# Optimization experiments

Hardware: AMD Instinct MI355X
Metric: run time of the kernel (lower is better)

## Reference

```python
import jax, jax.numpy as jnp
import numpy as np

JACCARD_THRESH = 0.5
NEGPOS_RATIO = 3
VAR = (0.1, 0.2)


def point_form(p):
    # center-size (cx,cy,w,h) -> corner (xmin,ymin,xmax,ymax)
    return jnp.concatenate([p[:, :2] - p[:, 2:] / 2, p[:, :2] + p[:, 2:] / 2], axis=1)


def jaccard(a, b):
    # a: [No,4] corner boxes, b: [Np,4] corner boxes -> IoU [No,Np]
    lt = jnp.maximum(a[:, None, :2], b[None, :, :2])
    rb = jnp.minimum(a[:, None, 2:], b[None, :, 2:])
    wh = jnp.clip(rb - lt, 0.0)
    inter = wh[..., 0] * wh[..., 1]
    area_a = ((a[:, 2] - a[:, 0]) * (a[:, 3] - a[:, 1]))[:, None]
    area_b = ((b[:, 2] - b[:, 0]) * (b[:, 3] - b[:, 1]))[None, :]
    return inter / (area_a + area_b - inter)


def encode(matched, priors):
    # matched: [Np,4] corner GT, priors: [Np,4] center-size
    g_cxcy = ((matched[:, :2] + matched[:, 2:]) / 2 - priors[:, :2]) / (VAR[0] * priors[:, 2:])
    g_wh = jnp.log((matched[:, 2:] - matched[:, :2]) / priors[:, 2:]) / VAR[1]
    return jnp.concatenate([g_cxcy, g_wh], axis=1)


def match_one(truths, labels, priors):
    # truths: [No,4], labels: [No], priors: [Np,4] center-size
    overlaps = jaccard(truths, point_form(priors))          # [No,Np]
    best_prior_idx = jnp.argmax(overlaps, axis=1)           # [No]
    best_truth_overlap = jnp.max(overlaps, axis=0)          # [Np]
    best_truth_idx = jnp.argmax(overlaps, axis=0)           # [Np]
    # each GT keeps its best prior (overlap forced to 2)
    best_truth_overlap = best_truth_overlap.at[best_prior_idx].set(2.0)
    best_truth_idx = best_truth_idx.at[best_prior_idx].set(jnp.arange(truths.shape[0]))
    matched = truths[best_truth_idx]                        # [Np,4]
    conf = labels[best_truth_idx].astype(jnp.int32) + 1     # background = 0
    conf = jnp.where(best_truth_overlap < JACCARD_THRESH, 0, conf)
    return encode(matched, priors), conf


def reference(loc_data, conf_data, dbox_list, targets):
    num_batch, num_dbox, num_classes = conf_data.shape
    truths = targets[:, :, :4]
    labels = targets[:, :, 4]
    loc_t, conf_t = jax.vmap(match_one, in_axes=(0, 0, None))(truths, labels, dbox_list)
    pos_mask = conf_t > 0                                   # [B,Np]
    # localization loss: SmoothL1 (beta=1), summed over positive dboxes
    diff = loc_data - loc_t
    ad = jnp.abs(diff)
    sl1 = jnp.where(ad < 1.0, 0.5 * diff * diff, ad - 0.5)
    loss_l = jnp.sum(sl1 * pos_mask[..., None].astype(sl1.dtype))
    # per-dbox cross entropy
    logp = jax.nn.log_softmax(conf_data, axis=-1)
    ce = -jnp.take_along_axis(logp, conf_t[..., None], axis=-1)[..., 0]  # [B,Np]
    # hard negative mining: rank (descending) of pos-zeroed CE via double argsort
    loss_c_hnm = jnp.where(pos_mask, 0.0, ce)
    loss_idx = jnp.argsort(-loss_c_hnm, axis=1)
    idx_rank = jnp.argsort(loss_idx, axis=1)
    num_pos = jnp.sum(pos_mask, axis=1, keepdims=True)      # [B,1]
    num_neg = jnp.minimum(num_pos * NEGPOS_RATIO, num_dbox)
    neg_mask = idx_rank < num_neg
    sel = jnp.logical_or(pos_mask, neg_mask)
    loss_c = jnp.sum(jnp.where(sel, ce, 0.0))
    N = jnp.sum(num_pos).astype(loss_l.dtype)
    return loss_l / N, loss_c / N


def setup_inputs() -> dict:
    key = jax.random.key(0)
    ks = jax.random.split(key, 7)
    B, Np, C, No = 128, 8732, 21, 16
    loc_data = jax.random.normal(ks[0], (B, Np, 4), dtype=jnp.float32) * 0.1
    conf_data = jax.random.normal(ks[1], (B, Np, C), dtype=jnp.float32)
    # default boxes in center-size form, w/h strictly positive
    cxcy = jax.random.uniform(ks[2], (Np, 2), minval=0.05, maxval=0.95)
    wh = jax.random.uniform(ks[3], (Np, 2), minval=0.05, maxval=0.5)
    dbox_list = jnp.concatenate([cxcy, wh], axis=1).astype(jnp.float32)
    # ground truth: valid corner-form boxes + class label in [0,20)
    gcxcy = jax.random.uniform(ks[4], (B, No, 2), minval=0.2, maxval=0.8)
    gwh = jax.random.uniform(ks[5], (B, No, 2), minval=0.05, maxval=0.3)
    boxes = jnp.concatenate([gcxcy - gwh / 2, gcxcy + gwh / 2], axis=-1)
    lab = jax.random.randint(ks[6], (B, No, 1), 0, C - 1).astype(jnp.float32)
    targets = jnp.concatenate([boxes, lab], axis=-1).astype(jnp.float32)
    return {"loc_data": loc_data, "conf_data": conf_data, "dbox_list": dbox_list, "targets": targets}
```

## Files before the change

### kernel.cpp

```cpp
#include <hip/hip_runtime.h>
#include <stdint.h>

#define TPB 256
#define SELTPB 1024
#define SELWAVES (SELTPB / 64)
#define MAXNO 64
#define NMB 16

__device__ __forceinline__ float sl1f(float d) {
    float ad = fabsf(d);
    return ad < 1.0f ? 0.5f * d * d : ad - 0.5f;
}

__device__ __forceinline__ float iou_pair(float tx1, float ty1, float tx2, float ty2, float ta,
                                          float px1, float py1, float px2, float py2, float pa) {
    float ltx = fmaxf(tx1, px1), lty = fmaxf(ty1, py1);
    float rbx = fminf(tx2, px2), rby = fminf(ty2, py2);
    float wx = fmaxf(rbx - ltx, 0.0f), wy = fmaxf(rby - lty, 0.0f);
    float inter = wx * wy;
    return inter / ((ta + pa) - inter);
}

template <int NO>
__global__ __launch_bounds__(256) void match_partial_kernel(
    const float* __restrict__ dbox, const float* __restrict__ targets,
    unsigned long long* __restrict__ pkeys, int Np, int No) {
    int b = blockIdx.y, mb = blockIdx.x;
    int tid = threadIdx.x;
    __shared__ float s_t[NO][5];
    __shared__ unsigned long long s_k[4][NO];
    if (tid < No) {
        const float* tr = targets + ((size_t)b * No + tid) * 5;
        float x1 = tr[0], y1 = tr[1], x2 = tr[2], y2 = tr[3];
        s_t[tid][0] = x1; s_t[tid][1] = y1; s_t[tid][2] = x2; s_t[tid][3] = y2;
        s_t[tid][4] = (x2 - x1) * (y2 - y1);
    }
    __syncthreads();
    int clen = (Np + NMB - 1) / NMB;
    int start = mb * clen;
    int end = start + clen;
    if (end > Np) end = Np;
    unsigned long long key[NO];
#pragma unroll
    for (int t = 0; t < NO; ++t) key[t] = 0ull;
    for (int p = start + tid; p < end; p += 256) {
        float4 pr = *reinterpret_cast<const float4*>(dbox + (size_t)p * 4);
        float px1 = pr.x - pr.z * 0.5f, py1 = pr.y - pr.w * 0.5f;
        float px2 = pr.x + pr.z * 0.5f, py2 = pr.y + pr.w * 0.5f;
        float pa = (px2 - px1) * (py2 - py1);
        unsigned lowp = 0xFFFFFFFFu - (unsigned)p;
#pragma unroll
        for (int t = 0; t < NO; ++t) {
            float iou = iou_pair(s_t[t][0], s_t[t][1], s_t[t][2], s_t[t][3], s_t[t][4],
                                 px1, py1, px2, py2, pa);
            unsigned long long k =
                (((unsigned long long)__float_as_uint(iou)) << 32) | (unsigned long long)lowp;
            if (k > key[t]) key[t] = k;
        }
    }
    int lane = tid & 63, wv = tid >> 6;
#pragma unroll
    for (int t = 0; t < NO; ++t) {
        unsigned long long k = key[t];
        for (int off = 32; off; off >>= 1) {
            unsigned long long o = __shfl_down(k, off);
            if (o > k) k = o;
        }
        if (lane == 0) s_k[wv][t] = k;
    }
    __syncthreads();
    if (tid < No) {
        unsigned long long m = s_k[0][tid];
#pragma unroll
        for (int w = 1; w < 4; ++w)
            if (s_k[w][tid] > m) m = s_k[w][tid];
        pkeys[((size_t)b * NMB + mb) * No + tid] = m;
    }
}

template <int CC>
__global__ __launch_bounds__(TPB) void main_kernel(
    const float* __restrict__ loc, const float* __restrict__ conf,
    const float* __restrict__ dbox, const float* __restrict__ targets,
    const unsigned long long* __restrict__ pkeys,
    float* __restrict__ v, float* __restrict__ part_l, float* __restrict__ part_c,
    int* __restrict__ part_n, int Np, int C, int No, int nchunk) {
    extern __shared__ float s_conf[];
    __shared__ float s_t[MAXNO][5];
    __shared__ float s_lab[MAXNO];
    __shared__ int s_ovr[MAXNO];
    __shared__ float s_red1[4];
    __shared__ float s_red2[4];
    __shared__ int s_redi[4];
    int b = blockIdx.y, chunk = blockIdx.x, tid = threadIdx.x;
    int p = chunk * TPB + tid;
    bool valid = p < Np;
    if (tid < No) {
        const float* tr = targets + ((size_t)b * No + tid) * 5;
        float x1 = tr[0], y1 = tr[1], x2 = tr[2], y2 = tr[3];
        s_t[tid][0] = x1; s_t[tid][1] = y1; s_t[tid][2] = x2; s_t[tid][3] = y2;
        s_t[tid][4] = (x2 - x1) * (y2 - y1);
        s_lab[tid] = tr[4];
        unsigned long long k = pkeys[((size_t)b * NMB + 0) * No + tid];
        for (int m = 1; m < NMB; ++m) {
            unsigned long long kk = pkeys[((size_t)b * NMB + m) * No + tid];
            if (kk > k) k = kk;
        }
        s_ovr[tid] = (int)(0xFFFFFFFFu - (unsigned)(k & 0xFFFFFFFFull));
    }
    int pbase = chunk * TPB;
    int cnt = Np - pbase;
    if (cnt > TPB) cnt = TPB;
    const float* cbase = conf + ((size_t)b * Np + (size_t)pbase) * C;
    {
        int ntot = cnt * C;
        int nv4 = ntot >> 2;
        const float4* c4 = reinterpret_cast<const float4*>(cbase);
        float4* s4 = reinterpret_cast<float4*>(s_conf);
        for (int i = tid; i < nv4; i += TPB) s4[i] = c4[i];
        for (int i = (nv4 << 2) + tid; i < ntot; i += TPB) s_conf[i] = cbase[i];
    }
    __syncthreads();

    float lossl = 0.0f, posce = 0.0f;
    int npos = 0;
    if (valid) {
        float4 pr = *reinterpret_cast<const float4*>(dbox + (size_t)p * 4);
        float px1 = pr.x - pr.z * 0.5f, py1 = pr.y - pr.w * 0.5f;
        float px2 = pr.x + pr.z * 0.5f, py2 = pr.y + pr.w * 0.5f;
        float pa = (px2 - px1) * (py2 - py1);
        float bov = -1.0f;
        int bidx = 0;
        for (int t = 0; t < No; ++t) {
            float iou = iou_pair(s_t[t][0], s_t[t][1], s_t[t][2], s_t[t][3], s_t[t][4],
                                 px1, py1, px2, py2, pa);
            if (iou > bov) { bov = iou; bidx = t; }
        }
        for (int t = 0; t < No; ++t)
            if (s_ovr[t] == p) { bidx = t; bov = 2.0f; }
        int ct = (bov < 0.5f) ? 0 : ((int)s_lab[bidx] + 1);
        float ce;
        if (CC > 0) {
            const float* crow = s_conf + tid * CC;
            float fr[CC > 0 ? CC : 1];
            float mx = -1e30f, fc = 0.0f;
#pragma unroll
            for (int j = 0; j < CC; ++j) {
                float x = crow[j];
                fr[j] = x;
                mx = fmaxf(mx, x);
                fc = (j == ct) ? x : fc;
            }
            float s = 0.0f;
#pragma unroll
            for (int j = 0; j < CC; ++j) s += __expf(fr[j] - mx);
            ce = __logf(s) + mx - fc;
        } else {
            const float* crow = s_conf + (size_t)tid * C;
            float mx = crow[0];
            for (int j = 1; j < C; ++j) mx = fmaxf(mx, crow[j]);
            float s = 0.0f;
            for (int j = 0; j < C; ++j) s += __expf(crow[j] - mx);
            ce = __logf(s) + mx - crow[ct];
        }
        bool pos = ct > 0;
        v[(size_t)b * Np + p] = pos ? 0.0f : ce;
        if (pos) {
            posce = ce;
            npos = 1;
            float mx1 = s_t[bidx][0], my1 = s_t[bidx][1], mx2 = s_t[bidx][2], my2 = s_t[bidx][3];
            float gcx = ((mx1 + mx2) * 0.5f - pr.x) / (0.1f * pr.z);
            float gcy = ((my1 + my2) * 0.5f - pr.y) / (0.1f * pr.w);
            float gw = __logf((mx2 - mx1) / pr.z) / 0.2f;
            float gh = __logf((my2 - my1) / pr.w) / 0.2f;
            float4 l4 = *reinterpret_cast<const float4*>(loc + ((size_t)b * Np + p) * 4);
            lossl = sl1f(l4.x - gcx) + sl1f(l4.y - gcy) + sl1f(l4.z - gw) + sl1f(l4.w - gh);
        }
    }
    float a1 = lossl, a2 = posce;
    int ni = npos;
    for (int off = 32; off; off >>= 1) {
        a1 += __shfl_down(a1, off);
        a2 += __shfl_down(a2, off);
        ni += __shfl_down(ni, off);
    }
    if ((tid & 63) == 0) {
        s_red1[tid >> 6] = a1;
        s_red2[tid >> 6] = a2;
        s_redi[tid >> 6] = ni;
    }
    __syncthreads();
    if (tid == 0) {
        part_l[(size_t)b * nchunk + chunk] = s_red1[0] + s_red1[1] + s_red1[2] + s_red1[3];
        part_c[(size_t)b * nchunk + chunk] = s_red2[0] + s_red2[1] + s_red2[2] + s_red2[3];
        part_n[(size_t)b * nchunk + chunk] = s_redi[0] + s_redi[1] + s_redi[2] + s_redi[3];
    }
}

__global__ __launch_bounds__(SELTPB) void select_kernel(
    const float* __restrict__ v, const float* __restrict__ pl,
    const float* __restrict__ pc, const int* __restrict__ pn,
    float* __restrict__ row_res, int Np, int nchunk, int negpos) {
    int b = blockIdx.x, tid = threadIdx.x;
    int lane = tid & 63, wv = tid >> 6;
    extern __shared__ unsigned sv[];
    __shared__ unsigned whist[SELWAVES][256];
    __shared__ unsigned suf[257];
    __shared__ float s_f[SELWAVES];
    __shared__ int s_dig, s_acc;
    __shared__ float s_lossl, s_posce;
    __shared__ int s_np;

    if (wv == 0) {
        float a = 0.0f, c = 0.0f;
        int n = 0;
        for (int i = lane; i < nchunk; i += 64) {
            a += pl[(size_t)b * nchunk + i];
            c += pc[(size_t)b * nchunk + i];
            n += pn[(size_t)b * nchunk + i];
        }
        for (int off = 32; off; off >>= 1) {
            a += __shfl_down(a, off);
            c += __shfl_down(c, off);
            n += __shfl_down(n, off);
        }
        if (lane == 0) { s_lossl = a; s_posce = c; s_np = n; }
    }
    {
        const float4* v4 = reinterpret_cast<const float4*>(v + (size_t)b * Np);
        int n4 = Np >> 2;
        for (int i = tid; i < n4; i += SELTPB) {
            float4 f = v4[i];
            uint4 u;
            u.x = __float_as_uint(f.x); u.y = __float_as_uint(f.y);
            u.z = __float_as_uint(f.z); u.w = __float_as_uint(f.w);
            *reinterpret_cast<uint4*>(&sv[i << 2]) = u;
        }
        for (int i = (n4 << 2) + tid; i < Np; i += SELTPB)
            sv[i] = __float_as_uint(v[(size_t)b * Np + i]);
    }
    __syncthreads();
    int npos = s_np;
    int K = npos * negpos;
    if (K > Np) K = Np;
    float lossc = s_posce;
    if (K > 0) {
        unsigned prefix = 0;
        int Krem = K;
        for (int shift = 24; shift >= 0; shift -= 8) {
            for (int i = tid; i < SELWAVES * 256; i += SELTPB)
                (&whist[0][0])[i] = 0;
            __syncthreads();
            for (int i = tid; i < Np; i += SELTPB) {
                unsigned u = sv[i];
                bool match = (shift == 24) || ((u >> (shift + 8)) == (prefix >> (shift + 8)));
                if (match) atomicAdd(&whist[wv][(u >> shift) & 0xFFu], 1u);
            }
            __syncthreads();
            if (tid < 256) {
                unsigned t = 0;
                for (int w = 0; w < SELWAVES; ++w) t += whist[w][tid];
                suf[tid] = t;
            }
            if (tid == 0) suf[256] = 0;
            __syncthreads();
            for (int off = 1; off < 256; off <<= 1) {
                unsigned add = 0;
                if (tid < 256 && tid + off < 256) add = suf[tid + off];
                __syncthreads();
                if (tid < 256) suf[tid] += add;
                __syncthreads();
            }
            if (tid < 256) {
                unsigned S = suf[tid];
                unsigned Snext = suf[tid + 1];
                if ((int)S >= Krem && (int)Snext < Krem) { s_dig = tid; s_acc = (int)Snext; }
            }
            __syncthreads();
            prefix |= ((unsigned)s_dig) << shift;
            Krem -= s_acc;
            __syncthreads();
        }
        float sum_gt = 0.0f;
        for (int i = tid; i < Np; i += SELTPB) {
            unsigned u = sv[i];
            if (u > prefix) sum_gt += __uint_as_float(u);
        }
        for (int off = 32; off; off >>= 1) sum_gt += __shfl_down(sum_gt, off);
        if (lane == 0) s_f[wv] = sum_gt;
        __syncthreads();
        if (tid == 0) {
            float t = 0.0f;
            for (int w = 0; w < SELWAVES; ++w) t += s_f[w];
            lossc += t + (float)Krem * __uint_as_float(prefix);
        }
    }
    if (tid == 0) {
        row_res[(size_t)b * 3 + 0] = s_lossl;
        row_res[(size_t)b * 3 + 1] = lossc;
        row_res[(size_t)b * 3 + 2] = (float)npos;
    }
}

__global__ __launch_bounds__(TPB) void finalize_kernel(
    const float* __restrict__ row_res, float* __restrict__ out, int B) {
    int tid = threadIdx.x;
    float l = 0, c = 0, n = 0;
    for (int i = tid; i < B; i += TPB) {
        l += row_res[(size_t)i * 3 + 0];
        c += row_res[(size_t)i * 3 + 1];
        n += row_res[(size_t)i * 3 + 2];
    }
    __shared__ float sl[4], sc[4], sn[4];
    for (int off = 32; off; off >>= 1) {
        l += __shfl_down(l, off);
        c += __shfl_down(c, off);
        n += __shfl_down(n, off);
    }
    int lane = tid & 63, w = tid >> 6;
    if (lane == 0) { sl[w] = l; sc[w] = c; sn[w] = n; }
    __syncthreads();
    if (tid == 0) {
        l = sl[0] + sl[1] + sl[2] + sl[3];
        c = sc[0] + sc[1] + sc[2] + sc[3];
        n = sn[0] + sn[1] + sn[2] + sn[3];
        out[0] = l / n;
        out[1] = c / n;
    }
}

extern "C" void kernel_launch(void* const* d_in, const int* in_sizes, int n_in,
                              void* d_out, int out_size, void* d_ws, size_t ws_size,
                              hipStream_t stream) {
    const float* loc = (const float*)d_in[0];
    const float* conf = (const float*)d_in[1];
    const float* dbox = (const float*)d_in[2];
    const float* targets = (const float*)d_in[3];

    int Np = in_sizes[2] / 4;
    int B = in_sizes[0] / (Np * 4);
    int C = in_sizes[1] / (B * Np);
    int No = in_sizes[3] / (B * 5);
    int nchunk = (Np + TPB - 1) / TPB;

    char* w = (char*)d_ws;
    unsigned long long* pkeys = (unsigned long long*)w;
    w += (size_t)B * NMB * No * sizeof(unsigned long long);
    float* v = (float*)w;
    w += (size_t)B * Np * sizeof(float);
    float* part_l = (float*)w;
    w += (size_t)B * nchunk * sizeof(float);
    float* part_c = (float*)w;
    w += (size_t)B * nchunk * sizeof(float);
    int* part_n = (int*)w;
    w += (size_t)B * nchunk * sizeof(int);
    float* row_res = (float*)w;

    dim3 mgrid(NMB, B);
    if (No == 16)
        match_partial_kernel<16><<<mgrid, 256, 0, stream>>>(dbox, targets, pkeys, Np, No);
    else
        match_partial_kernel<MAXNO><<<mgrid, 256, 0, stream>>>(dbox, targets, pkeys, Np, No);

    dim3 grid(nchunk, B);
    size_t lds_main = (size_t)TPB * C * sizeof(float);
    if (C == 21)
        main_kernel<21><<<grid, TPB, lds_main, stream>>>(loc, conf, dbox, targets, pkeys,
                                                         v, part_l, part_c, part_n, Np, C, No, nchunk);
    else
        main_kernel<0><<<grid, TPB, lds_main, stream>>>(loc, conf, dbox, targets, pkeys,
                                                        v, part_l, part_c, part_n, Np, C, No, nchunk);
    select_kernel<<<B, SELTPB, (size_t)Np * sizeof(float), stream>>>(v, part_l, part_c, part_n,
                                                                     row_res, Np, nchunk, 3);
    finalize_kernel<<<1, TPB, 0, stream>>>(row_res, (float*)d_out, B);
}
```

Before: 87.20 us.

## Precombine per-GT match keys in a tiny kernel and read box metadata uniformly

Adds a small combine kernel that reduces the per-chunk best-prior keys once per batch and writes a padded 8-float metadata record per ground-truth box. The main kernel no longer has every block re-reduce the 16 partial keys. Its IoU loop now reads box coordinates from global memory with block-uniform addresses instead of LDS, and folds the forced-match check into the same loop. A template specialisation on No lets the loop fully unroll. The cost is one extra kernel launch and reliance on scalar/cached global loads instead of shared memory.

```diff
diff --git a/kernel.cpp b/kernel.cpp
--- a/kernel.cpp
+++ b/kernel.cpp
@@ -78,17 +78,34 @@
     }
 }
 
-template <int CC>
+__global__ __launch_bounds__(64) void combine_kernel(
+    const unsigned long long* __restrict__ pkeys, const float* __restrict__ targets,
+    float* __restrict__ tmeta, int No) {
+    int b = blockIdx.x, t = threadIdx.x;
+    if (t >= No) return;
+    unsigned long long k = pkeys[((size_t)b * NMB + 0) * No + t];
+    for (int m = 1; m < NMB; ++m) {
+        unsigned long long kk = pkeys[((size_t)b * NMB + m) * No + t];
+        if (kk > k) k = kk;
+    }
+    const float* tr = targets + ((size_t)b * No + t) * 5;
+    float x1 = tr[0], y1 = tr[1], x2 = tr[2], y2 = tr[3];
+    float* tm = tmeta + ((size_t)b * MAXNO + t) * 8;
+    tm[0] = x1; tm[1] = y1; tm[2] = x2; tm[3] = y2;
+    tm[4] = (x2 - x1) * (y2 - y1);
+    tm[5] = tr[4];
+    tm[6] = __uint_as_float(0xFFFFFFFFu - (unsigned)(k & 0xFFFFFFFFull));
+    tm[7] = 0.0f;
+}
+
+template <int CC, int TNO>
 __global__ __launch_bounds__(TPB) void main_kernel(
     const float* __restrict__ loc, const float* __restrict__ conf,
-    const float* __restrict__ dbox, const float* __restrict__ targets,
-    const unsigned long long* __restrict__ pkeys,
+    const float* __restrict__ dbox, const float* __restrict__ tmeta,
     float* __restrict__ v, float* __restrict__ part_l, float* __restrict__ part_c,
     int* __restrict__ part_n, int Np, int C, int No, int nchunk) {
     extern __shared__ float s_conf[];
-    __shared__ float s_t[MAXNO][5];
-    __shared__ float s_lab[MAXNO];
-    __shared__ int s_ovr[MAXNO];
+    __shared__ float s_tb[MAXNO][5];
     __shared__ float s_red1[4];
     __shared__ float s_red2[4];
     __shared__ int s_redi[4];
@@ -96,17 +113,10 @@
     int p = chunk * TPB + tid;
     bool valid = p < Np;
     if (tid < No) {
-        const float* tr = targets + ((size_t)b * No + tid) * 5;
-        float x1 = tr[0], y1 = tr[1], x2 = tr[2], y2 = tr[3];
-        s_t[tid][0] = x1; s_t[tid][1] = y1; s_t[tid][2] = x2; s_t[tid][3] = y2;
-        s_t[tid][4] = (x2 - x1) * (y2 - y1);
-        s_lab[tid] = tr[4];
-        unsigned long long k = pkeys[((size_t)b * NMB + 0) * No + tid];
-        for (int m = 1; m < NMB; ++m) {
-            unsigned long long kk = pkeys[((size_t)b * NMB + m) * No + tid];
-            if (kk > k) k = kk;
-        }
-        s_ovr[tid] = (int)(0xFFFFFFFFu - (unsigned)(k & 0xFFFFFFFFull));
+        const float* tm = tmeta + ((size_t)b * MAXNO + tid) * 8;
+        s_tb[tid][0] = tm[0]; s_tb[tid][1] = tm[1];
+        s_tb[tid][2] = tm[2]; s_tb[tid][3] = tm[3];
+        s_tb[tid][4] = tm[5];
     }
     int pbase = chunk * TPB;
     int cnt = Np - pbase;
@@ -131,14 +141,27 @@
         float pa = (px2 - px1) * (py2 - py1);
         float bov = -1.0f;
         int bidx = 0;
-        for (int t = 0; t < No; ++t) {
-            float iou = iou_pair(s_t[t][0], s_t[t][1], s_t[t][2], s_t[t][3], s_t[t][4],
-                                 px1, py1, px2, py2, pa);
-            if (iou > bov) { bov = iou; bidx = t; }
-        }
-        for (int t = 0; t < No; ++t)
-            if (s_ovr[t] == p) { bidx = t; bov = 2.0f; }
-        int ct = (bov < 0.5f) ? 0 : ((int)s_lab[bidx] + 1);
+        int ovt = -1;
+        if (TNO > 0) {
+#pragma unroll
+            for (int t = 0; t < TNO; ++t) {
+                const float* tm = tmeta + ((size_t)b * MAXNO + t) * 8;
+                float iou = iou_pair(tm[0], tm[1], tm[2], tm[3], tm[4],
+                                     px1, py1, px2, py2, pa);
+                if (iou > bov) { bov = iou; bidx = t; }
+                if (__float_as_uint(tm[6]) == (unsigned)p) ovt = t;
+            }
+        } else {
+            for (int t = 0; t < No; ++t) {
+                const float* tm = tmeta + ((size_t)b * MAXNO + t) * 8;
+                float iou = iou_pair(tm[0], tm[1], tm[2], tm[3], tm[4],
+                                     px1, py1, px2, py2, pa);
+                if (iou > bov) { bov = iou; bidx = t; }
+                if (__float_as_uint(tm[6]) == (unsigned)p) ovt = t;
+            }
+        }
+        if (ovt >= 0) { bidx = ovt; bov = 2.0f; }
+        int ct = (bov < 0.5f) ? 0 : ((int)s_tb[bidx][4] + 1);
         float ce;
         if (CC > 0) {
             const float* crow = s_conf + tid * CC;
@@ -168,7 +191,8 @@
         if (pos) {
             posce = ce;
             npos = 1;
-            float mx1 = s_t[bidx][0], my1 = s_t[bidx][1], mx2 = s_t[bidx][2], my2 = s_t[bidx][3];
+            float mx1 = s_tb[bidx][0], my1 = s_tb[bidx][1];
+            float mx2 = s_tb[bidx][2], my2 = s_tb[bidx][3];
             float gcx = ((mx1 + mx2) * 0.5f - pr.x) / (0.1f * pr.z);
             float gcy = ((my1 + my2) * 0.5f - pr.y) / (0.1f * pr.w);
             float gw = __logf((mx2 - mx1) / pr.z) / 0.2f;
@@ -346,6 +370,8 @@
     char* w = (char*)d_ws;
     unsigned long long* pkeys = (unsigned long long*)w;
     w += (size_t)B * NMB * No * sizeof(unsigned long long);
+    float* tmeta = (float*)w;
+    w += (size_t)B * MAXNO * 8 * sizeof(float);
     float* v = (float*)w;
     w += (size_t)B * Np * sizeof(float);
     float* part_l = (float*)w;
@@ -362,14 +388,16 @@
     else
         match_partial_kernel<MAXNO><<<mgrid, 256, 0, stream>>>(dbox, targets, pkeys, Np, No);
 
+    combine_kernel<<<B, 64, 0, stream>>>(pkeys, targets, tmeta, No);
+
     dim3 grid(nchunk, B);
     size_t lds_main = (size_t)TPB * C * sizeof(float);
-    if (C == 21)
-        main_kernel<21><<<grid, TPB, lds_main, stream>>>(loc, conf, dbox, targets, pkeys,
-                                                         v, part_l, part_c, part_n, Np, C, No, nchunk);
+    if (C == 21 && No == 16)
+        main_kernel<21, 16><<<grid, TPB, lds_main, stream>>>(loc, conf, dbox, tmeta,
+                                                             v, part_l, part_c, part_n, Np, C, No, nchunk);
     else
-        main_kernel<0><<<grid, TPB, lds_main, stream>>>(loc, conf, dbox, targets, pkeys,
-                                                        v, part_l, part_c, part_n, Np, C, No, nchunk);
+        main_kernel<0, 0><<<grid, TPB, lds_main, stream>>>(loc, conf, dbox, tmeta,
+                                                           v, part_l, part_c, part_n, Np, C, No, nchunk);
     select_kernel<<<B, SELTPB, (size_t)Np * sizeof(float), stream>>>(v, part_l, part_c, part_n,
                                                                      row_res, Np, nchunk, 3);
     finalize_kernel<<<1, TPB, 0, stream>>>(row_res, (float*)d_out, B);
```

Result: slower. 89.04 us (+2.1%).
